# Kernel optimization log

Hardware: AMD Instinct MI355X
Metric: run time of the kernel (lower is better)

The kernel has to match this reference:

```python
import jax, jax.numpy as jnp
import numpy as np

V = 257        # vocab size (prime -> multiplicative inverses exist mod V)
B = 64         # batch
L = 1024       # sequence length
TEMPERATURE = 1.0


def one_hot_argmax(logits, temperature):
    # hard one-hot forward, softmax-temperature backward (straight-through)
    hard = jax.nn.one_hot(jnp.argmax(logits, axis=-1), logits.shape[-1], dtype=logits.dtype)
    soft = jax.nn.softmax(logits / temperature, axis=-1)
    return soft + jax.lax.stop_gradient(hard - soft)


def setup_inputs() -> dict:
    key = jax.random.key(0)
    k1, k2, k3 = jax.random.split(key, 3)
    idx = jax.random.randint(k1, (B, L), 0, V)
    x = jax.nn.one_hot(idx, V, dtype=jnp.float32)          # [B, L, V] hard one-hot
    W = jax.random.normal(k2, (V, 2 * V), jnp.float32) * 0.05
    b = jax.random.normal(k3, (2 * V,), jnp.float32) * 0.05
    # extended-Euclid inverse table (V prime -> Fermat: a^(V-2) mod V); inv(0):=0
    inv = np.array([0] + [pow(a, V - 2, V) for a in range(1, V)], dtype=np.int32)
    return {"x": x, "W": W, "b": b, "inv_table": jnp.asarray(inv)}


def reference(x, W, b, inv_table):
    dtype = x.dtype
    u = jnp.arange(V)
    # one_hot_minus: shift_matrix[u, v] = shift[(v - u) % V]
    minus_idx = (u[None, :] - u[:, None]) % V              # [V, V]
    # one_hot_multiply: for a != 0, scaled[a, u] = inputs[(u * inv(a)) % V]
    vidx = (u[None, :] * inv_table[:, None]) % V           # [V, V]
    notzero = (u != 0).astype(dtype)[None, :, None]        # zero out scale-by-0 row

    @jax.checkpoint
    def step(prev, x_t):
        # prev: [B, V] previous output one-hot; x_t: [B, V] current input one-hot
        net = prev @ W + b                                  # [B, 2V] causal masked layer
        loc_logits, scale_logits = jnp.split(net, 2, axis=-1)
        loc = one_hot_argmax(loc_logits, TEMPERATURE)       # [B, V]
        scale = one_hot_argmax(scale_logits, TEMPERATURE)   # [B, V]
        # multiplicative inverse of scale in one-hot space (non-differentiable, as in py_func)
        inv_scale = jax.nn.one_hot(inv_table[jnp.argmax(scale, axis=-1)], V, dtype=dtype)
        # (x_t - loc) % V in one-hot space: einsum('...v,...uv->...u') with rolled loc
        shifted = jnp.einsum('bv,buv->bu', x_t, loc[:, minus_idx])
        # (shifted * inv_scale) % V in one-hot space
        scaled = shifted[:, vidx] * notzero                 # [B, V, V]
        out = jnp.einsum('ba,bau->bu', inv_scale, scaled)   # [B, V]
        return out, out

    init = jnp.zeros((x.shape[0], V), dtype)
    _, ys = jax.lax.scan(step, init, jnp.swapaxes(x, 0, 1))  # scan over L
    return jnp.swapaxes(ys, 0, 1)                            # [B, L, V]
```

## Files before the change

### kernel.cpp

```cpp
#include <hip/hip_runtime.h>
#include <stdint.h>

#define V 257
#define NB 64
#define L 1024
#define ZERO_STATE 257
#define NSTATE 258
#define CHUNKS 32
#define CLEN 32
#define EXTRACT_BLOCKS 2048

typedef float f32x4 __attribute__((ext_vector_type(4)));

__device__ __forceinline__ int gstep(const uint32_t* __restrict__ tbl, int p, int x) {
    uint32_t e = tbl[p];
    int ia  = (int)(e >> 16);
    int loc = (int)(e & 0xffff);
    int s = x - loc;
    s += (s >> 31) & V;
    int n = s * ia;
    int m = (n & 255) - (n >> 8);
    m += (m >> 31) & V;
    return (ia == 0) ? ZERO_STATE : m;
}

__global__ void prep(const float* __restrict__ W, const float* __restrict__ bias,
                     const int* __restrict__ inv_table, const f32x4* __restrict__ x4,
                     uint32_t* __restrict__ gtable, uint16_t* __restrict__ xidx, int n4) {
    if (blockIdx.x < NSTATE) {
        int lane = threadIdx.x;
        if (lane >= 64) return;
        int p = blockIdx.x;
        const float* wrow = (p < V) ? (W + (size_t)p * (2 * V)) : nullptr;
        float bestL = -INFINITY; int idxL = 0;
        float bestS = -INFINITY; int idxS = 0;
        for (int j = lane; j < V; j += 64) {
            float vl = wrow ? (wrow[j] + bias[j]) : bias[j];
            float vs = wrow ? (wrow[V + j] + bias[V + j]) : bias[V + j];
            if (vl > bestL) { bestL = vl; idxL = j; }
            if (vs > bestS) { bestS = vs; idxS = j; }
        }
        for (int off = 32; off >= 1; off >>= 1) {
            float oL = __shfl_down(bestL, off); int oiL = __shfl_down(idxL, off);
            float oS = __shfl_down(bestS, off); int oiS = __shfl_down(idxS, off);
            if (oL > bestL || (oL == bestL && oiL < idxL)) { bestL = oL; idxL = oiL; }
            if (oS > bestS || (oS == bestS && oiS < idxS)) { bestS = oS; idxS = oiS; }
        }
        if (lane == 0) {
            int ia = inv_table[idxS];
            gtable[p] = (uint32_t)idxL | ((uint32_t)ia << 16);
        }
        return;
    }
    int stride = EXTRACT_BLOCKS * blockDim.x;
    for (int i = (blockIdx.x - NSTATE) * blockDim.x + threadIdx.x; i < n4; i += stride) {
        f32x4 v = x4[i];
        int j = i * 4;
        if (v.x == 1.0f) { int r = j / V;       xidx[r] = (uint16_t)(j     - r * V); }
        if (v.y == 1.0f) { int r = (j + 1) / V; xidx[r] = (uint16_t)(j + 1 - r * V); }
        if (v.z == 1.0f) { int r = (j + 2) / V; xidx[r] = (uint16_t)(j + 2 - r * V); }
        if (v.w == 1.0f) { int r = (j + 3) / V; xidx[r] = (uint16_t)(j + 3 - r * V); }
    }
}

__global__ void phase1(const uint32_t* __restrict__ gtable, const uint16_t* __restrict__ xidx,
                       uint16_t* __restrict__ f) {
    __shared__ uint32_t tbl[NSTATE];
    __shared__ uint16_t xs[CLEN];
    int bc = blockIdx.x;
    int b = bc / CHUNKS, c = bc % CHUNKS;
    int tid = threadIdx.x;
    for (int j = tid; j < NSTATE; j += 128) tbl[j] = gtable[j];
    if (tid < CLEN) xs[tid] = xidx[b * L + c * CLEN + tid];
    __syncthreads();
    int p0 = tid;
    int p1 = tid + 128;
    int p2 = (tid + 256 < NSTATE) ? tid + 256 : 0;
    #pragma unroll 4
    for (int k = 0; k < CLEN; ++k) {
        int x = xs[k];
        p0 = gstep(tbl, p0, x);
        p1 = gstep(tbl, p1, x);
        p2 = gstep(tbl, p2, x);
    }
    uint16_t* frow = f + (size_t)bc * NSTATE;
    frow[tid] = (uint16_t)p0;
    frow[tid + 128] = (uint16_t)p1;
    if (tid < 2) frow[tid + 256] = (uint16_t)p2;
}

__global__ void phase23(const uint32_t* __restrict__ gtable, const uint16_t* __restrict__ xidx,
                        const uint16_t* __restrict__ f, uint16_t* __restrict__ oidx) {
    __shared__ uint32_t tbl[NSTATE];
    __shared__ uint16_t fl[CHUNKS * NSTATE];
    __shared__ uint16_t xs[L];
    __shared__ uint16_t os[L];
    __shared__ uint16_t entry[CHUNKS];
    int b = blockIdx.x, tid = threadIdx.x;
    for (int j = tid; j < NSTATE; j += 256) tbl[j] = gtable[j];
    for (int j = tid; j < CHUNKS * NSTATE; j += 256) fl[j] = f[(size_t)b * CHUNKS * NSTATE + j];
    for (int j = tid; j < L; j += 256) xs[j] = xidx[b * L + j];
    __syncthreads();
    if (tid == 0) {
        int st = ZERO_STATE;
        for (int c = 0; c < CHUNKS; ++c) { entry[c] = (uint16_t)st; st = fl[c * NSTATE + st]; }
    }
    __syncthreads();
    if (tid < CHUNKS) {
        int p = entry[tid];
        int base = tid * CLEN;
        for (int k = 0; k < CLEN; ++k) {
            int x = xs[base + k];
            uint32_t e = tbl[p];
            int ia  = (int)(e >> 16);
            int loc = (int)(e & 0xffff);
            if (ia == 0) {
                os[base + k] = 0xFFFF;
                p = ZERO_STATE;
            } else {
                int s = x - loc;
                s += (s >> 31) & V;
                int n = s * ia;
                int m = (n & 255) - (n >> 8);
                m += (m >> 31) & V;
                os[base + k] = (uint16_t)m;
                p = m;
            }
        }
    }
    __syncthreads();
    for (int j = tid; j < L; j += 256) oidx[b * L + j] = os[j];
}

__global__ void write_out(const uint16_t* __restrict__ oidx, f32x4* __restrict__ out, int n4) {
    int stride = gridDim.x * blockDim.x;
    for (int i = blockIdx.x * blockDim.x + threadIdx.x; i < n4; i += stride) {
        int j = i * 4;
        int r = j / V;
        int c = j - r * V;
        int h0 = oidx[r];
        int h1 = (c + 3 >= V) ? oidx[r + 1] : h0;
        f32x4 v;
        int cc = c;
        v.x = (cc == h0) ? 1.0f : 0.0f; cc++;
        if (cc == V) { cc = 0; h0 = h1; }
        v.y = (cc == h0) ? 1.0f : 0.0f; cc++;
        if (cc == V) { cc = 0; h0 = h1; }
        v.z = (cc == h0) ? 1.0f : 0.0f; cc++;
        if (cc == V) { cc = 0; h0 = h1; }
        v.w = (cc == h0) ? 1.0f : 0.0f;
        out[i] = v;
    }
}

extern "C" void kernel_launch(void* const* d_in, const int* in_sizes, int n_in,
                              void* d_out, int out_size, void* d_ws, size_t ws_size,
                              hipStream_t stream) {
    const float* x    = (const float*)d_in[0];
    const float* W    = (const float*)d_in[1];
    const float* bias = (const float*)d_in[2];
    const int*   inv  = (const int*)d_in[3];

    uint8_t* ws = (uint8_t*)d_ws;
    uint32_t* gtable = (uint32_t*)ws;
    uint16_t* xidx   = (uint16_t*)(ws + 4096);
    uint16_t* oidx   = (uint16_t*)(ws + 4096 + NB * L * 2);
    uint16_t* f      = (uint16_t*)(ws + 4096 + 2 * NB * L * 2);

    int n4 = NB * L * V / 4;

    prep<<<NSTATE + EXTRACT_BLOCKS, 256, 0, stream>>>(W, bias, inv, (const f32x4*)x,
                                                      gtable, xidx, n4);
    phase1<<<NB * CHUNKS, 128, 0, stream>>>(gtable, xidx, f);
    phase23<<<NB, 256, 0, stream>>>(gtable, xidx, f, oidx);
    write_out<<<2048, 256, 0, stream>>>(oidx, (f32x4*)d_out, n4);
}
```

Baseline: 139.1 us.

## Fuse chunk replay with one-hot output write into per-chunk blocks

Merges the per-batch replay kernel and the separate output-writing kernel into one kernel launched with one block per (batch, chunk). Each block loads only the transition maps of the preceding chunks, composes them serially to find its entry state, replays its 32 steps, and writes its own slice of the one-hot output straight from shared memory. This removes one launch, the intermediate index buffer round trip, and the low-parallelism 64-block phase. In exchange, the entry-state composition is recomputed redundantly in every block, and later chunks load up to 31 map rows, so per-block work is uneven.

After: 138.1 us, median of 2. About the same (-0.8%).

```diff
diff --git a/kernel.cpp b/kernel.cpp
--- a/kernel.cpp
+++ b/kernel.cpp
@@ -9,6 +9,7 @@
 #define CHUNKS 32
 #define CLEN 32
 #define EXTRACT_BLOCKS 2048
+#define VECS_PER_CHUNK 2056
 
 typedef float f32x4 __attribute__((ext_vector_type(4)));
 
@@ -89,33 +90,34 @@
     if (tid < 2) frow[tid + 256] = (uint16_t)p2;
 }
 
-__global__ void phase23(const uint32_t* __restrict__ gtable, const uint16_t* __restrict__ xidx,
-                        const uint16_t* __restrict__ f, uint16_t* __restrict__ oidx) {
+__global__ void __launch_bounds__(256)
+replay_write(const uint32_t* __restrict__ gtable, const uint16_t* __restrict__ xidx,
+             const uint16_t* __restrict__ f, f32x4* __restrict__ out) {
     __shared__ uint32_t tbl[NSTATE];
-    __shared__ uint16_t fl[CHUNKS * NSTATE];
-    __shared__ uint16_t xs[L];
-    __shared__ uint16_t os[L];
-    __shared__ uint16_t entry[CHUNKS];
-    int b = blockIdx.x, tid = threadIdx.x;
+    __shared__ uint16_t fl[(CHUNKS - 1) * NSTATE];
+    __shared__ uint16_t xs[CLEN];
+    __shared__ uint16_t os[CLEN];
+    int b = blockIdx.x >> 5, c = blockIdx.x & 31;
+    int tid = threadIdx.x;
+
     for (int j = tid; j < NSTATE; j += 256) tbl[j] = gtable[j];
-    for (int j = tid; j < CHUNKS * NSTATE; j += 256) fl[j] = f[(size_t)b * CHUNKS * NSTATE + j];
-    for (int j = tid; j < L; j += 256) xs[j] = xidx[b * L + j];
+    int nfl = c * NSTATE;
+    const uint16_t* fb = f + (size_t)b * CHUNKS * NSTATE;
+    for (int j = tid; j < nfl; j += 256) fl[j] = fb[j];
+    if (tid < CLEN) xs[tid] = xidx[b * L + c * CLEN + tid];
     __syncthreads();
+
     if (tid == 0) {
         int st = ZERO_STATE;
-        for (int c = 0; c < CHUNKS; ++c) { entry[c] = (uint16_t)st; st = fl[c * NSTATE + st]; }
-    }
-    __syncthreads();
-    if (tid < CHUNKS) {
-        int p = entry[tid];
-        int base = tid * CLEN;
+        for (int i = 0; i < c; ++i) st = fl[i * NSTATE + st];
+        int p = st;
         for (int k = 0; k < CLEN; ++k) {
-            int x = xs[base + k];
+            int x = xs[k];
             uint32_t e = tbl[p];
             int ia  = (int)(e >> 16);
             int loc = (int)(e & 0xffff);
             if (ia == 0) {
-                os[base + k] = 0xFFFF;
+                os[k] = 0xFFFF;
                 p = ZERO_STATE;
             } else {
                 int s = x - loc;
@@ -123,25 +125,22 @@
                 int n = s * ia;
                 int m = (n & 255) - (n >> 8);
                 m += (m >> 31) & V;
-                os[base + k] = (uint16_t)m;
+                os[k] = (uint16_t)m;
                 p = m;
             }
         }
     }
     __syncthreads();
-    for (int j = tid; j < L; j += 256) oidx[b * L + j] = os[j];
-}
 
-__global__ void write_out(const uint16_t* __restrict__ oidx, f32x4* __restrict__ out, int n4) {
-    int stride = gridDim.x * blockDim.x;
-    for (int i = blockIdx.x * blockDim.x + threadIdx.x; i < n4; i += stride) {
-        int j = i * 4;
-        int r = j / V;
-        int c = j - r * V;
-        int h0 = oidx[r];
-        int h1 = (c + 3 >= V) ? oidx[r + 1] : h0;
+    f32x4* obase = out + ((size_t)(b * L + c * CLEN) * V) / 4;
+    for (int i = tid; i < VECS_PER_CHUNK; i += 256) {
+        int e = i * 4;
+        int r = e / V;
+        int col = e - r * V;
+        int h0 = os[r];
+        int h1 = (col + 3 >= V) ? os[r + 1] : h0;
         f32x4 v;
-        int cc = c;
+        int cc = col;
         v.x = (cc == h0) ? 1.0f : 0.0f; cc++;
         if (cc == V) { cc = 0; h0 = h1; }
         v.y = (cc == h0) ? 1.0f : 0.0f; cc++;
@@ -149,7 +148,7 @@
         v.z = (cc == h0) ? 1.0f : 0.0f; cc++;
         if (cc == V) { cc = 0; h0 = h1; }
         v.w = (cc == h0) ? 1.0f : 0.0f;
-        out[i] = v;
+        obase[i] = v;
     }
 }
 
@@ -164,14 +163,12 @@
     uint8_t* ws = (uint8_t*)d_ws;
     uint32_t* gtable = (uint32_t*)ws;
     uint16_t* xidx   = (uint16_t*)(ws + 4096);
-    uint16_t* oidx   = (uint16_t*)(ws + 4096 + NB * L * 2);
-    uint16_t* f      = (uint16_t*)(ws + 4096 + 2 * NB * L * 2);
+    uint16_t* f      = (uint16_t*)(ws + 4096 + NB * L * 2);
 
     int n4 = NB * L * V / 4;
 
     prep<<<NSTATE + EXTRACT_BLOCKS, 256, 0, stream>>>(W, bias, inv, (const f32x4*)x,
                                                       gtable, xidx, n4);
     phase1<<<NB * CHUNKS, 128, 0, stream>>>(gtable, xidx, f);
-    phase23<<<NB, 256, 0, stream>>>(gtable, xidx, f, oidx);
-    write_out<<<2048, 256, 0, stream>>>(oidx, (f32x4*)d_out, n4);
+    replay_write<<<NB * CHUNKS, 256, 0, stream>>>(gtable, xidx, f, (f32x4*)d_out);
 }
```
